# Kernel tuning notes

Measured on AMD Instinct MI355X. Metric: run time of the kernel, lower is better.

Reference implementation:

```python
import jax, jax.numpy as jnp
import numpy as np

BS = 4  # gating blocksize


def setup_inputs() -> dict:
    key = jax.random.key(0)
    k1, k2, k3 = jax.random.split(key, 3)
    batch, rows, width, cols = 8, 2048, 4096, 4096
    X = jax.random.normal(k1, (batch, rows, width), dtype=jnp.float32)
    W = jax.random.normal(k2, (width, cols), dtype=jnp.float32)
    G = jax.random.normal(k3, (batch, width // BS, cols // BS), dtype=jnp.float32)
    return {"X": X, "W": W, "G": G}


def _gmm(X, W, G):
    # Y[b,r,c] = sum_k X[b,r,k] * W[k,c] * G[b, k//BS, c//BS]
    b = X.shape[0]
    # expand block gates to elementwise resolution
    Gf = jnp.repeat(jnp.repeat(G, BS, axis=1), BS, axis=2)  # (b, width, cols)
    # per-batch gated weight, then batched GEMM
    return jnp.einsum('brk,kc,bkc->brc', X, W, Gf)


def reference(X, W, G):
    Y = _gmm(X, W, G)
    s = Y.sum()
    return s * s
```

## Files before the change

kernel.cpp:

```cpp
#include <hip/hip_runtime.h>

#define BATCH 8
#define ROWS  2048
#define WIDTH 4096
#define COLS  4096
#define KB    1024
#define CBV   1024
#define ZPART 32
#define RCH   64

typedef float f32x4 __attribute__((ext_vector_type(4)));

__global__ __launch_bounds__(256) void colsum_kernel(const f32x4* __restrict__ X,
                                                     f32x4* __restrict__ part) {
    const int k4 = blockIdx.x * 256 + threadIdx.x;
    const int b  = blockIdx.y;
    const int z  = blockIdx.z;

    const f32x4* p = X + (size_t)(b * ROWS + z * RCH) * (WIDTH / 4) + k4;
    f32x4 a = {0.f, 0.f, 0.f, 0.f};
#pragma unroll 8
    for (int r = 0; r < RCH; ++r) {
        f32x4 v = p[(size_t)r * (WIDTH / 4)];
        a.x += v.x; a.y += v.y; a.z += v.z; a.w += v.w;
    }
    part[((size_t)(z * BATCH + b) << 10) + k4] = a;
}

__global__ __launch_bounds__(256) void gated_kernel(const f32x4* __restrict__ Wv,
                                                    const f32x4* __restrict__ Gv,
                                                    const f32x4* __restrict__ part,
                                                    float* __restrict__ blocksum) {
    const int t  = threadIdx.x;
    const int kb = blockIdx.x;
    const int lane = t & 63, wv = t >> 6;

    f32x4 v = part[((size_t)((t >> 3) * BATCH + (t & 7)) << 10) + kb];

    f32x4 w[4][4];
#pragma unroll
    for (int j = 0; j < 4; ++j)
#pragma unroll
        for (int m = 0; m < 4; ++m)
            w[j][m] = Wv[(size_t)(4 * kb + j) * CBV + 4 * t + m];

    f32x4 g[8];
#pragma unroll
    for (int b = 0; b < 8; ++b)
        g[b] = Gv[((size_t)(b * KB + kb) << 8) + t];

#pragma unroll
    for (int o = 8; o < 64; o <<= 1) {
        v.x += __shfl_xor(v.x, o, 64);
        v.y += __shfl_xor(v.y, o, 64);
        v.z += __shfl_xor(v.z, o, 64);
        v.w += __shfl_xor(v.w, o, 64);
    }
    __shared__ f32x4 ldsx[4][8];
    if (lane < 8) ldsx[wv][lane] = v;
    __syncthreads();
    f32x4 xs4[8];
#pragma unroll
    for (int b = 0; b < 8; ++b)
        xs4[b] = (ldsx[0][b] + ldsx[1][b]) + (ldsx[2][b] + ldsx[3][b]);

    float w4[4][4];
#pragma unroll
    for (int j = 0; j < 4; ++j)
#pragma unroll
        for (int m = 0; m < 4; ++m)
            w4[j][m] = (w[j][m].x + w[j][m].y) + (w[j][m].z + w[j][m].w);

    float acc = 0.f;
#pragma unroll
    for (int b = 0; b < 8; ++b) {
        float in0 = 0.f, in1 = 0.f, in2 = 0.f, in3 = 0.f;
#pragma unroll
        for (int j = 0; j < 4; ++j) {
            const float xv = (j == 0) ? xs4[b].x : (j == 1) ? xs4[b].y
                                                 : (j == 2) ? xs4[b].z : xs4[b].w;
            in0 += xv * w4[j][0];
            in1 += xv * w4[j][1];
            in2 += xv * w4[j][2];
            in3 += xv * w4[j][3];
        }
        acc += g[b].x * in0 + g[b].y * in1 + g[b].z * in2 + g[b].w * in3;
    }

#pragma unroll
    for (int o = 1; o < 64; o <<= 1) acc += __shfl_xor(acc, o, 64);
    __shared__ float ldss[4];
    if (lane == 0) ldss[wv] = acc;
    __syncthreads();
    if (t == 0) blocksum[kb] = (ldss[0] + ldss[1]) + (ldss[2] + ldss[3]);
}

__global__ __launch_bounds__(256) void final_kernel(const f32x4* __restrict__ bs4,
                                                    float* __restrict__ out) {
    f32x4 v = bs4[threadIdx.x];
    float acc = (v.x + v.y) + (v.z + v.w);
    __shared__ float red[256];
    red[threadIdx.x] = acc;
    __syncthreads();
    for (int o = 128; o > 0; o >>= 1) {
        if (threadIdx.x < o) red[threadIdx.x] += red[threadIdx.x + o];
        __syncthreads();
    }
    if (threadIdx.x == 0) {
        float s = red[0];
        out[0] = s * s;
    }
}

extern "C" void kernel_launch(void* const* d_in, const int* in_sizes, int n_in,
                              void* d_out, int out_size, void* d_ws, size_t ws_size,
                              hipStream_t stream) {
    const float* X = (const float*)d_in[0];
    const float* W = (const float*)d_in[1];
    const float* G = (const float*)d_in[2];
    float* out = (float*)d_out;

    float* part     = (float*)d_ws;
    float* blocksum = part + (size_t)ZPART * BATCH * WIDTH;

    dim3 g1(WIDTH / 4 / 256, BATCH, ZPART);
    colsum_kernel<<<g1, 256, 0, stream>>>((const f32x4*)X, (f32x4*)part);

    gated_kernel<<<KB, 256, 0, stream>>>((const f32x4*)W, (const f32x4*)G,
                                         (const f32x4*)part, blocksum);

    final_kernel<<<1, 256, 0, stream>>>((const f32x4*)blocksum, out);
}
```

Baseline: 81.83 us.

## Overlap X column sums with gated weight reduction in one interleaved launch

```diff
diff --git a/kernel.cpp b/kernel.cpp
--- a/kernel.cpp
+++ b/kernel.cpp
@@ -11,105 +11,100 @@
 
 typedef float f32x4 __attribute__((ext_vector_type(4)));
 
-__global__ __launch_bounds__(256) void colsum_kernel(const f32x4* __restrict__ X,
-                                                     f32x4* __restrict__ part) {
-    const int k4 = blockIdx.x * 256 + threadIdx.x;
-    const int b  = blockIdx.y;
-    const int z  = blockIdx.z;
+__global__ __launch_bounds__(256) void fused_kernel(const f32x4* __restrict__ X,
+                                                    const f32x4* __restrict__ Wv,
+                                                    const f32x4* __restrict__ Gv,
+                                                    f32x4* __restrict__ part,
+                                                    float* __restrict__ wg) {
+    const int t = threadIdx.x;
+    if (!(blockIdx.x & 1)) {
+        const int s  = blockIdx.x >> 1;
+        const int k4 = (s & 3) * 256 + t;
+        const int b  = (s >> 2) & 7;
+        const int z  = s >> 5;
 
-    const f32x4* p = X + (size_t)(b * ROWS + z * RCH) * (WIDTH / 4) + k4;
-    f32x4 a = {0.f, 0.f, 0.f, 0.f};
+        const f32x4* p = X + (size_t)(b * ROWS + z * RCH) * (WIDTH / 4) + k4;
+        f32x4 a = {0.f, 0.f, 0.f, 0.f};
 #pragma unroll 8
-    for (int r = 0; r < RCH; ++r) {
-        f32x4 v = p[(size_t)r * (WIDTH / 4)];
-        a.x += v.x; a.y += v.y; a.z += v.z; a.w += v.w;
+        for (int r = 0; r < RCH; ++r) {
+            f32x4 v = p[(size_t)r * (WIDTH / 4)];
+            a.x += v.x; a.y += v.y; a.z += v.z; a.w += v.w;
+        }
+        part[((size_t)(z * BATCH + b) << 10) + k4] = a;
+    } else {
+        const int kb = blockIdx.x >> 1;
+        const int lane = t & 63, wv = t >> 6;
+
+        f32x4 w[4][4];
+#pragma unroll
+        for (int j = 0; j < 4; ++j)
+#pragma unroll
+            for (int m = 0; m < 4; ++m)
+                w[j][m] = Wv[(size_t)(4 * kb + j) * CBV + 4 * t + m];
+
+        f32x4 g[8];
+#pragma unroll
+        for (int b = 0; b < 8; ++b)
+            g[b] = Gv[((size_t)(b * KB + kb) << 8) + t];
+
+        float w4[4][4];
+#pragma unroll
+        for (int j = 0; j < 4; ++j)
+#pragma unroll
+            for (int m = 0; m < 4; ++m)
+                w4[j][m] = (w[j][m].x + w[j][m].y) + (w[j][m].z + w[j][m].w);
+
+        float acc[8][4];
+#pragma unroll
+        for (int b = 0; b < 8; ++b)
+#pragma unroll
+            for (int j = 0; j < 4; ++j)
+                acc[b][j] = g[b].x * w4[j][0] + g[b].y * w4[j][1] +
+                            g[b].z * w4[j][2] + g[b].w * w4[j][3];
+
+        __shared__ float lds[4][32];
+#pragma unroll
+        for (int v = 0; v < 32; ++v) {
+            float x = acc[v >> 2][v & 3];
+#pragma unroll
+            for (int o = 1; o < 64; o <<= 1) x += __shfl_xor(x, o, 64);
+            if (lane == 0) lds[wv][v] = x;
+        }
+        __syncthreads();
+        if (t < 32) {
+            float r = (lds[0][t] + lds[1][t]) + (lds[2][t] + lds[3][t]);
+            wg[(size_t)(t >> 2) * WIDTH + 4 * kb + (t & 3)] = r;
+        }
     }
-    part[((size_t)(z * BATCH + b) << 10) + k4] = a;
 }
 
-__global__ __launch_bounds__(256) void gated_kernel(const f32x4* __restrict__ Wv,
-                                                    const f32x4* __restrict__ Gv,
-                                                    const f32x4* __restrict__ part,
-                                                    float* __restrict__ blocksum) {
-    const int t  = threadIdx.x;
-    const int kb = blockIdx.x;
-    const int lane = t & 63, wv = t >> 6;
-
-    f32x4 v = part[((size_t)((t >> 3) * BATCH + (t & 7)) << 10) + kb];
-
-    f32x4 w[4][4];
-#pragma unroll
-    for (int j = 0; j < 4; ++j)
-#pragma unroll
-        for (int m = 0; m < 4; ++m)
-            w[j][m] = Wv[(size_t)(4 * kb + j) * CBV + 4 * t + m];
-
-    f32x4 g[8];
-#pragma unroll
-    for (int b = 0; b < 8; ++b)
-        g[b] = Gv[((size_t)(b * KB + kb) << 8) + t];
-
-#pragma unroll
-    for (int o = 8; o < 64; o <<= 1) {
-        v.x += __shfl_xor(v.x, o, 64);
-        v.y += __shfl_xor(v.y, o, 64);
-        v.z += __shfl_xor(v.z, o, 64);
-        v.w += __shfl_xor(v.w, o, 64);
-    }
-    __shared__ f32x4 ldsx[4][8];
-    if (lane < 8) ldsx[wv][lane] = v;
-    __syncthreads();
-    f32x4 xs4[8];
-#pragma unroll
-    for (int b = 0; b < 8; ++b)
-        xs4[b] = (ldsx[0][b] + ldsx[1][b]) + (ldsx[2][b] + ldsx[3][b]);
-
-    float w4[4][4];
-#pragma unroll
-    for (int j = 0; j < 4; ++j)
-#pragma unroll
-        for (int m = 0; m < 4; ++m)
-            w4[j][m] = (w[j][m].x + w[j][m].y) + (w[j][m].z + w[j][m].w);
-
+__global__ __launch_bounds__(256) void dot_kernel(const f32x4* __restrict__ part,
+                                                  const f32x4* __restrict__ wgv,
+                                                  float* __restrict__ partial) {
+    const int z = blockIdx.x;
+    const f32x4* pz = part + ((size_t)z * BATCH << 10);
     float acc = 0.f;
 #pragma unroll
-    for (int b = 0; b < 8; ++b) {
-        float in0 = 0.f, in1 = 0.f, in2 = 0.f, in3 = 0.f;
-#pragma unroll
-        for (int j = 0; j < 4; ++j) {
-            const float xv = (j == 0) ? xs4[b].x : (j == 1) ? xs4[b].y
-                                                 : (j == 2) ? xs4[b].z : xs4[b].w;
-            in0 += xv * w4[j][0];
-            in1 += xv * w4[j][1];
-            in2 += xv * w4[j][2];
-            in3 += xv * w4[j][3];
-        }
-        acc += g[b].x * in0 + g[b].y * in1 + g[b].z * in2 + g[b].w * in3;
+    for (int rep = 0; rep < BATCH * 1024 / 256; ++rep) {
+        const int i = rep * 256 + threadIdx.x;
+        f32x4 a = pz[i], b = wgv[i];
+        acc += a.x * b.x + a.y * b.y + a.z * b.z + a.w * b.w;
     }
-
 #pragma unroll
     for (int o = 1; o < 64; o <<= 1) acc += __shfl_xor(acc, o, 64);
-    __shared__ float ldss[4];
-    if (lane == 0) ldss[wv] = acc;
+    __shared__ float lds[4];
+    const int lane = threadIdx.x & 63, wv = threadIdx.x >> 6;
+    if (lane == 0) lds[wv] = acc;
     __syncthreads();
-    if (t == 0) blocksum[kb] = (ldss[0] + ldss[1]) + (ldss[2] + ldss[3]);
+    if (threadIdx.x == 0) partial[z] = (lds[0] + lds[1]) + (lds[2] + lds[3]);
 }
 
-__global__ __launch_bounds__(256) void final_kernel(const f32x4* __restrict__ bs4,
+__global__ __launch_bounds__(64) void square_kernel(const float* __restrict__ partial,
                                                     float* __restrict__ out) {
-    f32x4 v = bs4[threadIdx.x];
-    float acc = (v.x + v.y) + (v.z + v.w);
-    __shared__ float red[256];
-    red[threadIdx.x] = acc;
-    __syncthreads();
-    for (int o = 128; o > 0; o >>= 1) {
-        if (threadIdx.x < o) red[threadIdx.x] += red[threadIdx.x + o];
-        __syncthreads();
-    }
-    if (threadIdx.x == 0) {
-        float s = red[0];
-        out[0] = s * s;
-    }
+    float v = (threadIdx.x < ZPART) ? partial[threadIdx.x] : 0.f;
+#pragma unroll
+    for (int o = 1; o < 64; o <<= 1) v += __shfl_xor(v, o, 64);
+    if (threadIdx.x == 0) out[0] = v * v;
 }
 
 extern "C" void kernel_launch(void* const* d_in, const int* in_sizes, int n_in,
@@ -120,14 +115,14 @@
     const float* G = (const float*)d_in[2];
     float* out = (float*)d_out;
 
-    float* part     = (float*)d_ws;
-    float* blocksum = part + (size_t)ZPART * BATCH * WIDTH;
+    float* part    = (float*)d_ws;
+    float* wg      = part + (size_t)ZPART * BATCH * WIDTH;
+    float* partial = wg + (size_t)BATCH * WIDTH;
 
-    dim3 g1(WIDTH / 4 / 256, BATCH, ZPART);
-    colsum_kernel<<<g1, 256, 0, stream>>>((const f32x4*)X, (f32x4*)part);
+    fused_kernel<<<2048, 256, 0, stream>>>((const f32x4*)X, (const f32x4*)W,
+                                           (const f32x4*)G, (f32x4*)part, wg);
 
-    gated_kernel<<<KB, 256, 0, stream>>>((const f32x4*)W, (const f32x4*)G,
-                                         (const f32x4*)part, blocksum);
+    dot_kernel<<<ZPART, 256, 0, stream>>>((const f32x4*)part, (const f32x4*)wg, partial);
 
-    final_kernel<<<1, 256, 0, stream>>>((const f32x4*)blocksum, out);
+    square_kernel<<<1, 64, 0, stream>>>(partial, out);
 }
```

After: 79.70 us. -2.6%, faster.
